# Optimization experiments

Measured on AMD Instinct MI355X. Metric: run time of the kernel, lower is better.

## Reference

```python
import jax, jax.numpy as jnp
import numpy as np

EPS_LN = 1e-5

def _layernorm(x, g, b):
    mu = x.mean(-1, keepdims=True)
    var = ((x - mu) ** 2).mean(-1, keepdims=True)
    return (x - mu) / jnp.sqrt(var + EPS_LN) * g + b


def setup_inputs() -> dict:
    key = jax.random.key(0)
    B, N, D, H = 4, 2048, 256, 4
    hid = int(D * 2.0)
    ks = jax.random.split(key, 12)
    x = jax.random.normal(ks[0], (B, N, D), jnp.float32)
    Au = jax.random.uniform(ks[1], (N, N)) < 0.004
    A = jnp.logical_or(Au, Au.T)
    A = A.at[jnp.arange(N), jnp.arange(N)].set(False)
    Af = A.astype(jnp.float32)
    deg = Af.sum(axis=1)
    L = jnp.diag(deg) - Af                      # graph Laplacian (N,N), PSD
    adjacency = Af + jnp.eye(N, dtype=jnp.float32)  # self loops so no empty softmax rows
    s = lambda k, sh, f: jax.random.normal(k, sh, jnp.float32) * f
    sc = 1.0 / np.sqrt(D)
    Wc = s(ks[2], (D, D), sc); bc = jnp.zeros((D,), jnp.float32)
    Wq = s(ks[3], (D, D), sc); Wk = s(ks[4], (D, D), sc); Wv = s(ks[5], (D, D), sc)
    Wo = s(ks[6], (D, D), sc); bo = jnp.zeros((D,), jnp.float32)
    W1 = s(ks[7], (D, hid), sc); b1 = jnp.zeros((hid,), jnp.float32)
    W2 = s(ks[8], (hid, D), 1.0 / np.sqrt(hid)); b2 = jnp.zeros((D,), jnp.float32)
    g1 = jnp.ones((D,), jnp.float32); be1 = jnp.zeros((D,), jnp.float32)
    g2 = jnp.ones((D,), jnp.float32); be2 = jnp.zeros((D,), jnp.float32)
    g3 = jnp.ones((D,), jnp.float32); be3 = jnp.zeros((D,), jnp.float32)
    return dict(x=x, L=L, adjacency=adjacency, Wc=Wc, bc=bc, g1=g1, be1=be1,
                Wq=Wq, Wk=Wk, Wv=Wv, Wo=Wo, bo=bo, g2=g2, be2=be2,
                W1=W1, b1=b1, W2=W2, b2=b2, g3=g3, be3=be3)


def reference(x, L, adjacency, Wc, bc, g1, be1, Wq, Wk, Wv, Wo, bo,
              g2, be2, W1, b1, W2, b2, g3, be3):
    B, N, D = x.shape
    H = 4
    hd = D // H
    # --- LaplacianConv: normalize L to eigenvalues in [-1, 1] ---
    eig = jnp.linalg.eigvalsh(L)               # ascending
    lam_max = eig[-1] + 1e-8
    L_norm = 2.0 * L / lam_max - jnp.eye(N, dtype=L.dtype)
    # per-channel matmul in torch == single propagation L_norm @ x
    xp = jnp.einsum('mn,bnf->bmf', L_norm, x)
    h = xp @ Wc + bc
    h = _layernorm(h, g1, be1)
    h = jax.nn.relu(h)
    x1 = h + x                                  # residual (in_dim == out_dim)
    # --- adjacency-masked multi-head attention ---
    q = (x1 @ Wq).reshape(B, N, H, hd).transpose(0, 2, 1, 3)  # (B,H,N,hd)
    k = (x1 @ Wk).reshape(B, N, H, hd).transpose(0, 2, 1, 3)
    v = (x1 @ Wv).reshape(B, N, H, hd).transpose(0, 2, 1, 3)
    scores = jnp.einsum('bhnd,bhmd->bhnm', q, k) / np.sqrt(hd).astype(np.float32)
    scores = jnp.where(adjacency[None, None] > 0, scores, jnp.float32(-1e9))
    attn = jax.nn.softmax(scores, axis=-1)
    o = jnp.einsum('bhnm,bhmd->bhnd', attn, v)
    o = o.transpose(0, 2, 1, 3).reshape(B, N, D)
    o = o @ Wo + bo
    x2 = _layernorm(x1 + o, g2, be2)
    # --- MLP ---
    m = jax.nn.gelu(x2 @ W1 + b1, approximate=False) @ W2 + b2
    return _layernorm(x2 + m, g3, be3)
```

## Files before the change

### kernel.cpp

```cpp
#include <hip/hip_runtime.h>
#include <math.h>

typedef __bf16 bf16;
typedef bf16 bf16x8 __attribute__((ext_vector_type(8)));
typedef float f32x4 __attribute__((ext_vector_type(4)));

#define LDS_PAD 40
#define SENT 2048
#define LANCZOS_M 12

__global__ __launch_bounds__(256) void k_pre(
    const float* __restrict__ Wc, const float* __restrict__ Wq, const float* __restrict__ Wk,
    const float* __restrict__ Wv, const float* __restrict__ Wo, const float* __restrict__ W1,
    const float* __restrict__ W2, const float* __restrict__ x, const float* __restrict__ adj,
    bf16* __restrict__ WcT, bf16* __restrict__ WqT, bf16* __restrict__ WkT,
    bf16* __restrict__ WvT, bf16* __restrict__ WoT, bf16* __restrict__ W1T,
    bf16* __restrict__ W2T, bf16* __restrict__ xT,
    int* __restrict__ cnt, unsigned short* __restrict__ cols)
{
    __shared__ float tile[32][33];
    int z = blockIdx.z;
    if (z == 11) {
        int flat = blockIdx.y * 16 + blockIdx.x;
        if (flat >= 512) return;
        int row = flat * 4 + (threadIdx.x >> 6);
        int lane = threadIdx.x & 63;
        int base = 0;
        for (int c0 = 0; c0 < 2048; c0 += 64) {
            float a = adj[(long)row * 2048 + c0 + lane];
            unsigned long long m = __ballot(a != 0.0f);
            if (a != 0.0f) {
                int pos = base + __popcll(m & ((1ull << lane) - 1ull));
                if (pos < 64) cols[(long)row * 64 + pos] = (unsigned short)(c0 + lane);
            }
            base += __popcll(m);
        }
        int c = base < 64 ? base : 64;
        if (lane >= c) cols[(long)row * 64 + lane] = (unsigned short)SENT;
        if (lane == 0) cnt[row] = c;
        return;
    }
    const float* src; bf16* dst; int R, C;
    switch (z) {
        case 0: src = Wc; dst = WcT; R = 256; C = 256; break;
        case 1: src = Wq; dst = WqT; R = 256; C = 256; break;
        case 2: src = Wk; dst = WkT; R = 256; C = 256; break;
        case 3: src = Wv; dst = WvT; R = 256; C = 256; break;
        case 4: src = Wo; dst = WoT; R = 256; C = 256; break;
        case 5: src = W1; dst = W1T; R = 256; C = 512; break;
        case 6: src = W2; dst = W2T; R = 512; C = 256; break;
        default: {
            int b = z - 7;
            src = x + (long)b * 2048 * 256; dst = xT + (long)b * 256 * 2048;
            R = 2048; C = 256;
        }
    }
    int c0 = blockIdx.x * 32, r0 = blockIdx.y * 32;
    if (c0 >= C || r0 >= R) return;
    int tx = threadIdx.x & 31, ty = threadIdx.x >> 5;
#pragma unroll
    for (int j = 0; j < 4; ++j)
        tile[ty + 8 * j][tx] = src[(long)(r0 + ty + 8 * j) * C + c0 + tx];
    __syncthreads();
#pragma unroll
    for (int j = 0; j < 4; ++j)
        dst[(long)(c0 + ty + 8 * j) * R + r0 + tx] = (bf16)tile[tx][ty + 8 * j];
}

__global__ __launch_bounds__(1024) void k_main(
    const int* __restrict__ cnt, const unsigned short* __restrict__ cols, float* __restrict__ lamOut,
    const float* __restrict__ L, const bf16* __restrict__ xT, float* __restrict__ xp0f)
{
    __shared__ float va[2064], vb[2064];
    __shared__ float redf[16], redf2[16];
    __shared__ int   redi[16];
    __shared__ float bcast, bcast2;
    __shared__ float alphaA[LANCZOS_M], betaA[LANCZOS_M];
    __shared__ bf16 As[64 * LDS_PAD];
    __shared__ bf16 Bs[256 * LDS_PAD];

    int t = threadIdx.x;
    if (blockIdx.x != 0) {
        int bx = blockIdx.x - 1;
        int rowBlk = (bx & 31) * 64;
        int z  = (bx >> 5) & 3;
        int ks = bx >> 7;
        long kbase = (long)ks * 1024;
        const bf16* BT = xT + (long)z * 256 * 2048;
        int w = t >> 6, lane = t & 63;
        int q = lane >> 4, l15 = lane & 15;
        int wm = w & 3, wn = w >> 2;

        f32x4 acc[4];
#pragma unroll
        for (int i = 0; i < 4; ++i) acc[i] = (f32x4){0.0f, 0.0f, 0.0f, 0.0f};

        int ar = t >> 4, ac = (t & 15) * 2;
        int br = t >> 2, bc = (t & 3) * 8;
        const float* Ap = L + (long)(rowBlk + ar) * 2048 + kbase + ac;
        const bf16* Bp = BT + (long)br * 2048 + kbase + bc;
        float2 fA = *(const float2*)Ap;
        uint4  rB = *(const uint4*)Bp;
        for (int kt = 0; kt < 1024; kt += 32) {
            __syncthreads();
            {
                union { bf16 h[2]; unsigned u; } pk;
                pk.h[0] = (bf16)fA.x; pk.h[1] = (bf16)fA.y;
                *(unsigned*)&As[ar * LDS_PAD + ac] = pk.u;
            }
            *(uint4*)&Bs[br * LDS_PAD + bc] = rB;
            __syncthreads();
            if (kt + 32 < 1024) {
                fA = *(const float2*)(Ap + kt + 32);
                rB = *(const uint4*)(Bp + kt + 32);
            }
            bf16x8 a = *(const bf16x8*)&As[(wm * 16 + l15) * LDS_PAD + q * 8];
#pragma unroll
            for (int nt = 0; nt < 4; ++nt) {
                bf16x8 b = *(const bf16x8*)&Bs[((wn * 4 + nt) * 16 + l15) * LDS_PAD + q * 8];
                acc[nt] = __builtin_amdgcn_mfma_f32_16x16x32_bf16(a, b, acc[nt], 0, 0, 0);
            }
        }
        long zRow = (long)ks * 8192 + (long)z * 2048 + rowBlk + wm * 16 + q * 4;
#pragma unroll
        for (int nt = 0; nt < 4; ++nt) {
            int col = (wn * 4 + nt) * 16 + l15;
#pragma unroll
            for (int r = 0; r < 4; ++r)
                xp0f[(zRow + r) * 256 + col] = acc[nt][r];
        }
        return;
    }
    int wid = t >> 6, lane = t & 63;
    int r0 = t, r1 = t + 1024;
    int c0 = cnt[r0], c1 = cnt[r1];
    int p0 = (c0 + 7) & ~7, p1 = (c1 + 7) & ~7;

    uint4 cr0[8], cr1[8];
#pragma unroll
    for (int j = 0; j < 8; ++j) {
        cr0[j] = ((const uint4*)(cols + (long)r0 * 64))[j];
        cr1[j] = ((const uint4*)(cols + (long)r1 * 64))[j];
    }

    int md = max(c0, c1);
#pragma unroll
    for (int off = 32; off >= 1; off >>= 1) md = max(md, __shfl_xor(md, off));
    if (lane == 0) redi[wid] = md;
    __syncthreads();
    if (t == 0) {
        int m = 0;
        for (int i = 0; i < 16; ++i) m = max(m, redi[i]);
        bcast = (float)(2 * (m - 1)) + 1.0f;
    }
    for (int i = t; i < 2048; i += 1024) {
        unsigned u = (unsigned)i * 2654435761u;
        u ^= u >> 16; u *= 2246822519u; u ^= u >> 13;
        float mag = 0.5f + (float)((u >> 9) & 1023) * (1.0f / 1024.0f);
        va[i] = (u & 1) ? mag : -mag;
    }
    if (t == 0) { va[SENT] = 0.0f; vb[SENT] = 0.0f; }
    __syncthreads();
    float hiBound = bcast;

    float d0 = va[r0], d1 = va[r1];
    float pz = d0 * d0 + d1 * d1;
#pragma unroll
    for (int off = 32; off >= 1; off >>= 1) pz += __shfl_xor(pz, off);
    if (lane == 0) redf[wid] = pz;
    __syncthreads();
    if (t == 0) { float s = 0; for (int i = 0; i < 16; ++i) s += redf[i]; bcast = s; }
    __syncthreads();
    float sc = rsqrtf(fmaxf(bcast, 1e-30f));
    d0 *= sc; d1 *= sc;
    va[r0] = d0; va[r1] = d1;
    __syncthreads();

    float* cur = va; float* nxt = vb;
    float bp = 0.0f;
    float p0r = 0.0f, p1r = 0.0f;
    for (int it = 0; it < LANCZOS_M; ++it) {
        float sum0 = 0.0f, sum1 = 0.0f;
#pragma unroll
        for (int j = 0; j < 8; ++j)
            if (j * 8 < p0) {
                uint4 q = cr0[j];
                sum0 += cur[q.x & 0xffff] + cur[q.x >> 16] + cur[q.y & 0xffff] + cur[q.y >> 16]
                      + cur[q.z & 0xffff] + cur[q.z >> 16] + cur[q.w & 0xffff] + cur[q.w >> 16];
            }
#pragma unroll
        for (int j = 0; j < 8; ++j)
            if (j * 8 < p1) {
                uint4 q = cr1[j];
                sum1 += cur[q.x & 0xffff] + cur[q.x >> 16] + cur[q.y & 0xffff] + cur[q.y >> 16]
                      + cur[q.z & 0xffff] + cur[q.z >> 16] + cur[q.w & 0xffff] + cur[q.w >> 16];
            }
        float u0 = (float)c0 * d0 - sum0 - bp * p0r;
        float u1 = (float)c1 * d1 - sum1 - bp * p1r;
        float puv = u0 * d0 + u1 * d1;
        float puu = u0 * u0 + u1 * u1;
#pragma unroll
        for (int off = 32; off >= 1; off >>= 1) {
            puv += __shfl_xor(puv, off);
            puu += __shfl_xor(puu, off);
        }
        if (lane == 0) { redf[wid] = puv; redf2[wid] = puu; }
        __syncthreads();
        if (t == 0) {
            float sv = 0, su = 0;
            for (int i = 0; i < 16; ++i) { sv += redf[i]; su += redf2[i]; }
            float b = sqrtf(fmaxf(su - sv * sv, 1e-24f));
            alphaA[it] = sv; betaA[it] = b;
            bcast = sv; bcast2 = b;
        }
        __syncthreads();
        float alpha = bcast, beta = bcast2;
        float invb = 1.0f / beta;
        float w0 = u0 - alpha * d0, w1 = u1 - alpha * d1;
        p0r = d0; p1r = d1;
        d0 = w0 * invb; d1 = w1 * invb;
        nxt[r0] = d0; nxt[r1] = d1;
        __syncthreads();
        bp = beta;
        float* tmp = cur; cur = nxt; nxt = tmp;
    }

    if (t < 64) {
        float aa[LANCZOS_M], b2[LANCZOS_M];
#pragma unroll
        for (int i = 0; i < LANCZOS_M; ++i) { aa[i] = alphaA[i]; b2[i] = betaA[i] * betaA[i]; }
        float lo = 0.0f, hi = hiBound;
        for (int round = 0; round < 4; ++round) {
            float step = (hi - lo) * (1.0f / 65.0f);
            float xm = lo + step * (float)(lane + 1);
            float dd = aa[0] - xm;
            int neg = dd < 0.0f ? 1 : 0;
#pragma unroll
            for (int i = 1; i < LANCZOS_M; ++i) {
                float ad = fmaxf(fabsf(dd), 1e-12f);
                dd = (dd < 0.0f) ? -ad : ad;
                dd = aa[i] - xm - b2[i - 1] / dd;
                neg += dd < 0.0f ? 1 : 0;
            }
            unsigned long long mb = __ballot(neg >= LANCZOS_M);
            if (mb == 0ull) {
                lo = lo + step * 64.0f;
            } else {
                int fl = (int)(__ffsll((long long)mb) - 1);
                hi = lo + step * (float)(fl + 1);
                lo = lo + step * (float)fl;
            }
        }
        if (lane == 0) lamOut[0] = 0.5f * (lo + hi) + 1e-8f;
    }
}

template <int TA, int EPI>
__global__ __launch_bounds__(256) void k_gemm(
    const bf16* __restrict__ A0, const float* __restrict__ Apa, const float* __restrict__ Apb,
    const float* __restrict__ Aaux, const bf16* __restrict__ BTg,
    float* __restrict__ outF, bf16* __restrict__ outB,
    const float* __restrict__ bias, const float* __restrict__ resid,
    const float* __restrict__ gam, const float* __restrict__ bet,
    const float* __restrict__ lamPtr,
    int K, long aZ, long btZ, long outZrows, int ldOut)
{
    __shared__ bf16 As[64 * LDS_PAD];
    __shared__ bf16 Bs[256 * LDS_PAD];

    int tid = threadIdx.x;
    int w = tid >> 6, lane = tid & 63;
    int q = lane >> 4, l15 = lane & 15;
    int rowBlk = blockIdx.x * 64;
    int colB = blockIdx.y * 256;
    const bf16* BT = BTg + (long)blockIdx.z * btZ + (long)blockIdx.y * 256 * (long)K;

    float s2 = 0.0f;
    if (TA == 2) s2 = 2.0f / lamPtr[0];

    f32x4 acc[16];
#pragma unroll
    for (int i = 0; i < 16; ++i) acc[i] = (f32x4){0.0f, 0.0f, 0.0f, 0.0f};

    int ar = tid >> 2, ac = (tid & 3) * 8;
    long abase = (long)(rowBlk + ar) * K + ac;
    const bf16* A = A0 + (long)blockIdx.z * aZ;
    const bf16* Bp = BT + (long)tid * K;

    uint4 aR;
    float4 pa0, pa1, pb0, pb1, xa0, xa1;
    uint4 bR0, bR1, bR2, bR3;
    if (TA == 1) {
        aR = *(const uint4*)(A + abase);
    } else {
        pa0 = *(const float4*)(Apa + abase);  pa1 = *(const float4*)(Apa + abase + 4);
        pb0 = *(const float4*)(Apb + abase);  pb1 = *(const float4*)(Apb + abase + 4);
        xa0 = *(const float4*)(Aaux + abase); xa1 = *(const float4*)(Aaux + abase + 4);
    }
    bR0 = ((const uint4*)Bp)[0]; bR1 = ((const uint4*)Bp)[1];
    bR2 = ((const uint4*)Bp)[2]; bR3 = ((const uint4*)Bp)[3];

    for (int kt = 0; kt < K; kt += 32) {
        __syncthreads();
        if (TA == 1) {
            *(uint4*)&As[ar * LDS_PAD + ac] = aR;
        } else {
            float pa[8] = {pa0.x, pa0.y, pa0.z, pa0.w, pa1.x, pa1.y, pa1.z, pa1.w};
            float pb[8] = {pb0.x, pb0.y, pb0.z, pb0.w, pb1.x, pb1.y, pb1.z, pb1.w};
            float xa[8] = {xa0.x, xa0.y, xa0.z, xa0.w, xa1.x, xa1.y, xa1.z, xa1.w};
            union { bf16 h[8]; uint4 u; } pk;
#pragma unroll
            for (int j = 0; j < 8; ++j) pk.h[j] = (bf16)(s2 * (pa[j] + pb[j]) - xa[j]);
            *(uint4*)&As[ar * LDS_PAD + ac] = pk.u;
        }
        {
            bf16* d = &Bs[tid * LDS_PAD];
            *(uint4*)(d + 0)  = bR0;
            *(uint4*)(d + 8)  = bR1;
            *(uint4*)(d + 16) = bR2;
            *(uint4*)(d + 24) = bR3;
        }
        __syncthreads();
        if (kt + 32 < K) {
            long nb = abase + kt + 32;
            if (TA == 1) {
                aR = *(const uint4*)(A + nb);
            } else {
                pa0 = *(const float4*)(Apa + nb);  pa1 = *(const float4*)(Apa + nb + 4);
                pb0 = *(const float4*)(Apb + nb);  pb1 = *(const float4*)(Apb + nb + 4);
                xa0 = *(const float4*)(Aaux + nb); xa1 = *(const float4*)(Aaux + nb + 4);
            }
            const bf16* p = Bp + kt + 32;
            bR0 = ((const uint4*)p)[0]; bR1 = ((const uint4*)p)[1];
            bR2 = ((const uint4*)p)[2]; bR3 = ((const uint4*)p)[3];
        }
        bf16x8 a = *(const bf16x8*)&As[(w * 16 + l15) * LDS_PAD + q * 8];
#pragma unroll
        for (int nt = 0; nt < 16; ++nt) {
            bf16x8 b = *(const bf16x8*)&Bs[(nt * 16 + l15) * LDS_PAD + q * 8];
            acc[nt] = __builtin_amdgcn_mfma_f32_16x16x32_bf16(a, b, acc[nt], 0, 0, 0);
        }
    }

    long zRow = (long)blockIdx.z * outZrows + rowBlk + w * 16 + q * 4;

    if (EPI == 0) {
#pragma unroll
        for (int nt = 0; nt < 16; ++nt) {
            int col = colB + nt * 16 + l15;
#pragma unroll
            for (int r = 0; r < 4; ++r)
                outB[(zRow + r) * (long)ldOut + col] = (bf16)acc[nt][r];
        }
        return;
    }
    if (EPI == 3) {
#pragma unroll
        for (int nt = 0; nt < 16; ++nt) {
            int col = colB + nt * 16 + l15;
            float bi = bias[col];
#pragma unroll
            for (int r = 0; r < 4; ++r) {
                float v = acc[nt][r] + bi;
                float g = 0.5f * v * (1.0f + erff(v * 0.70710678118654752440f));
                outB[(zRow + r) * (long)ldOut + col] = (bf16)g;
            }
        }
        return;
    }
    float s[4] = {0, 0, 0, 0}, sq[4] = {0, 0, 0, 0};
#pragma unroll
    for (int nt = 0; nt < 16; ++nt) {
        int col = colB + nt * 16 + l15;
        float bi = bias[col];
#pragma unroll
        for (int r = 0; r < 4; ++r) {
            float v = acc[nt][r] + bi;
            if (EPI == 2) v += resid[(zRow + r) * 256 + col];
            acc[nt][r] = v;
            s[r] += v; sq[r] += v * v;
        }
    }
#pragma unroll
    for (int off = 1; off <= 8; off <<= 1) {
#pragma unroll
        for (int r = 0; r < 4; ++r) { s[r] += __shfl_xor(s[r], off); sq[r] += __shfl_xor(sq[r], off); }
    }
    float mean[4], rstd[4];
#pragma unroll
    for (int r = 0; r < 4; ++r) {
        mean[r] = s[r] * (1.0f / 256.0f);
        float var = sq[r] * (1.0f / 256.0f) - mean[r] * mean[r];
        rstd[r] = rsqrtf(var + 1e-5f);
    }
#pragma unroll
    for (int nt = 0; nt < 16; ++nt) {
        int col = colB + nt * 16 + l15;
        float gc = gam[col], bc2 = bet[col];
#pragma unroll
        for (int r = 0; r < 4; ++r) {
            float v = (acc[nt][r] - mean[r]) * rstd[r] * gc + bc2;
            if (EPI == 1) v = fmaxf(v, 0.0f) + resid[(zRow + r) * 256 + col];
            long oi = (zRow + r) * (long)ldOut + col;
            outF[oi] = v;
            if (outB) outB[oi] = (bf16)v;
        }
    }
}

__global__ __launch_bounds__(256) void k_attn(const bf16* __restrict__ qg, const bf16* __restrict__ kg,
                                              const bf16* __restrict__ vg, bf16* __restrict__ og,
                                              const int* __restrict__ cnt, const unsigned short* __restrict__ cols)
{
    __shared__ unsigned short sc[64];
    __shared__ float sp[4][64];
    int row = blockIdx.x;
    int b = row >> 11, i = row & 2047;
    int tid = threadIdx.x, h = tid >> 6, lane = tid & 63;
    int c = cnt[i];
    if (tid < 64) sc[tid] = cols[(long)i * 64 + tid];
    __syncthreads();
    long qoff = (long)row * 256 + h * 64 + lane;
    float qd = (float)qg[qoff];
    long kvBase = (long)b * 2048;
    for (int j = 0; j < c; ++j) {
        int col = sc[j];
        float kd = (float)kg[(kvBase + col) * 256 + h * 64 + lane];
        float p = qd * kd;
#pragma unroll
        for (int off = 32; off >= 1; off >>= 1) p += __shfl_xor(p, off);
        if (lane == 0) sp[h][j] = p * 0.125f;
    }
    __syncthreads();
    float sj = (lane < c) ? sp[h][lane] : -3.0e38f;
    float mx = sj;
#pragma unroll
    for (int off = 32; off >= 1; off >>= 1) mx = fmaxf(mx, __shfl_xor(mx, off));
    float e = (lane < c) ? __expf(sj - mx) : 0.0f;
    float ssum = e;
#pragma unroll
    for (int off = 32; off >= 1; off >>= 1) ssum += __shfl_xor(ssum, off);
    if (lane < c) sp[h][lane] = e / ssum;
    __syncthreads();
    float acc = 0.0f;
    for (int j = 0; j < c; ++j) {
        int col = sc[j];
        acc += sp[h][j] * (float)vg[(kvBase + col) * 256 + h * 64 + lane];
    }
    og[qoff] = (bf16)acc;
}

extern "C" void kernel_launch(void* const* d_in, const int* in_sizes, int n_in,
                              void* d_out, int out_size, void* d_ws, size_t ws_size,
                              hipStream_t stream)
{
    const float* x   = (const float*)d_in[0];
    const float* L   = (const float*)d_in[1];
    const float* adj = (const float*)d_in[2];
    const float* Wc  = (const float*)d_in[3];
    const float* bc  = (const float*)d_in[4];
    const float* g1  = (const float*)d_in[5];
    const float* be1 = (const float*)d_in[6];
    const float* Wq  = (const float*)d_in[7];
    const float* Wk  = (const float*)d_in[8];
    const float* Wv  = (const float*)d_in[9];
    const float* Wo  = (const float*)d_in[10];
    const float* bo  = (const float*)d_in[11];
    const float* g2  = (const float*)d_in[12];
    const float* be2 = (const float*)d_in[13];
    const float* W1  = (const float*)d_in[14];
    const float* b1  = (const float*)d_in[15];
    const float* W2  = (const float*)d_in[16];
    const float* b2  = (const float*)d_in[17];
    const float* g3  = (const float*)d_in[18];
    const float* be3 = (const float*)d_in[19];
    float* out = (float*)d_out;

    char* ws = (char*)d_ws;
    size_t off = 0;
    auto alloc = [&](size_t bytes) -> void* {
        void* p = ws + off;
        off = (off + bytes + 255) & ~(size_t)255;
        return p;
    };
    float* lam           = (float*)alloc(256);
    int* cnt             = (int*)alloc(2048 * 4);
    unsigned short* cols = (unsigned short*)alloc(2048 * 64 * 2);
    bf16* WcT = (bf16*)alloc(65536 * 2);
    bf16* WqT = (bf16*)alloc(65536 * 2);
    bf16* WkT = (bf16*)alloc(65536 * 2);
    bf16* WvT = (bf16*)alloc(65536 * 2);
    bf16* WoT = (bf16*)alloc(65536 * 2);
    bf16* W1T = (bf16*)alloc(131072 * 2);
    bf16* W2T = (bf16*)alloc(131072 * 2);
    bf16* xT  = (bf16*)alloc((size_t)4 * 256 * 2048 * 2);
    float* xp0f = (float*)alloc((size_t)2 * 8192 * 256 * 4);
    float* x1f = (float*)alloc((size_t)8192 * 256 * 4);
    bf16* x1b  = (bf16*)alloc((size_t)8192 * 256 * 2);
    bf16* qb   = (bf16*)alloc((size_t)3 * 8192 * 256 * 2);
    bf16* ob   = (bf16*)alloc((size_t)8192 * 256 * 2);
    float* x2f = (float*)alloc((size_t)8192 * 256 * 4);
    bf16* x2b  = (bf16*)alloc((size_t)8192 * 256 * 2);
    bf16* m1   = (bf16*)alloc((size_t)8192 * 512 * 2);
    (void)in_sizes; (void)n_in; (void)out_size; (void)ws_size;

    dim3 blk(256);
    k_pre<<<dim3(16, 64, 12), blk, 0, stream>>>(Wc, Wq, Wk, Wv, Wo, W1, W2, x, adj,
                                                WcT, WqT, WkT, WvT, WoT, W1T, W2T, xT, cnt, cols);
    k_main<<<dim3(257), dim3(1024), 0, stream>>>(cnt, cols, lam, L, xT, xp0f);
    k_gemm<2, 1><<<dim3(128, 1, 1), blk, 0, stream>>>(
        nullptr, xp0f, xp0f + (size_t)8192 * 256, x, WcT, x1f, x1b, bc, x, g1, be1, lam,
        256, 0L, 0L, 0L, 256);
    k_gemm<1, 0><<<dim3(128, 1, 3), blk, 0, stream>>>(
        x1b, nullptr, nullptr, nullptr, WqT, nullptr, qb, nullptr, nullptr, nullptr, nullptr, nullptr,
        256, 0L, 65536L, 8192L, 256);
    bf16* kb  = qb + (size_t)8192 * 256;
    bf16* vb2 = qb + (size_t)2 * 8192 * 256;
    k_attn<<<dim3(8192), blk, 0, stream>>>(qb, kb, vb2, ob, cnt, cols);
    k_gemm<1, 2><<<dim3(128, 1, 1), blk, 0, stream>>>(
        ob, nullptr, nullptr, nullptr, WoT, x2f, x2b, bo, x1f, g2, be2, nullptr,
        256, 0L, 0L, 0L, 256);
    k_gemm<1, 3><<<dim3(128, 2, 1), blk, 0, stream>>>(
        x2b, nullptr, nullptr, nullptr, W1T, nullptr, m1, b1, nullptr, nullptr, nullptr, nullptr,
        256, 0L, 0L, 0L, 512);
    k_gemm<1, 2><<<dim3(128, 1, 1), blk, 0, stream>>>(
        m1, nullptr, nullptr, nullptr, W2T, out, nullptr, b2, x2f, g3, be3, nullptr,
        512, 0L, 0L, 0L, 256);
}
```

Measured before the change: 384.7 us.

## Halve GEMM row tile to 32 and split columns across warps

The GEMM tile shrinks from 64 to 32 rows per block, and the four warps are arranged 2x2 (row half by column half) instead of each owning 16 rows across all 256 columns. The grid doubles to 256 blocks so more of the GPU's compute units get work on these small GEMMs. Row statistics for the fused layernorm are now combined across the two column-half warps through shared memory plus an extra barrier. The cost is that each block reloads the full 256-column B tile for only 32 rows, doubling B traffic, with smaller A loads.

Result: faster. 368.5 us (-4.2%).

```diff
diff --git a/kernel.cpp b/kernel.cpp
--- a/kernel.cpp
+++ b/kernel.cpp
@@ -265,37 +265,39 @@
     const float* __restrict__ lamPtr,
     int K, long aZ, long btZ, long outZrows, int ldOut)
 {
-    __shared__ bf16 As[64 * LDS_PAD];
+    __shared__ bf16 As[32 * LDS_PAD];
     __shared__ bf16 Bs[256 * LDS_PAD];
+    __shared__ float sL[2][32], sqL[2][32];
 
     int tid = threadIdx.x;
     int w = tid >> 6, lane = tid & 63;
     int q = lane >> 4, l15 = lane & 15;
-    int rowBlk = blockIdx.x * 64;
+    int wm = w & 1, wn = w >> 1;
+    int rowBlk = blockIdx.x * 32;
     int colB = blockIdx.y * 256;
     const bf16* BT = BTg + (long)blockIdx.z * btZ + (long)blockIdx.y * 256 * (long)K;
 
     float s2 = 0.0f;
     if (TA == 2) s2 = 2.0f / lamPtr[0];
 
-    f32x4 acc[16];
-#pragma unroll
-    for (int i = 0; i < 16; ++i) acc[i] = (f32x4){0.0f, 0.0f, 0.0f, 0.0f};
-
-    int ar = tid >> 2, ac = (tid & 3) * 8;
+    f32x4 acc[8];
+#pragma unroll
+    for (int i = 0; i < 8; ++i) acc[i] = (f32x4){0.0f, 0.0f, 0.0f, 0.0f};
+
+    int ar = tid >> 3, ac = (tid & 7) * 4;
     long abase = (long)(rowBlk + ar) * K + ac;
     const bf16* A = A0 + (long)blockIdx.z * aZ;
     const bf16* Bp = BT + (long)tid * K;
 
-    uint4 aR;
-    float4 pa0, pa1, pb0, pb1, xa0, xa1;
+    uint2 aR;
+    float4 pa0, pb0, xa0;
     uint4 bR0, bR1, bR2, bR3;
     if (TA == 1) {
-        aR = *(const uint4*)(A + abase);
+        aR = *(const uint2*)(A + abase);
     } else {
-        pa0 = *(const float4*)(Apa + abase);  pa1 = *(const float4*)(Apa + abase + 4);
-        pb0 = *(const float4*)(Apb + abase);  pb1 = *(const float4*)(Apb + abase + 4);
-        xa0 = *(const float4*)(Aaux + abase); xa1 = *(const float4*)(Aaux + abase + 4);
+        pa0 = *(const float4*)(Apa + abase);
+        pb0 = *(const float4*)(Apb + abase);
+        xa0 = *(const float4*)(Aaux + abase);
     }
     bR0 = ((const uint4*)Bp)[0]; bR1 = ((const uint4*)Bp)[1];
     bR2 = ((const uint4*)Bp)[2]; bR3 = ((const uint4*)Bp)[3];
@@ -303,15 +305,15 @@
     for (int kt = 0; kt < K; kt += 32) {
         __syncthreads();
         if (TA == 1) {
-            *(uint4*)&As[ar * LDS_PAD + ac] = aR;
+            *(uint2*)&As[ar * LDS_PAD + ac] = aR;
         } else {
-            float pa[8] = {pa0.x, pa0.y, pa0.z, pa0.w, pa1.x, pa1.y, pa1.z, pa1.w};
-            float pb[8] = {pb0.x, pb0.y, pb0.z, pb0.w, pb1.x, pb1.y, pb1.z, pb1.w};
-            float xa[8] = {xa0.x, xa0.y, xa0.z, xa0.w, xa1.x, xa1.y, xa1.z, xa1.w};
-            union { bf16 h[8]; uint4 u; } pk;
-#pragma unroll
-            for (int j = 0; j < 8; ++j) pk.h[j] = (bf16)(s2 * (pa[j] + pb[j]) - xa[j]);
-            *(uint4*)&As[ar * LDS_PAD + ac] = pk.u;
+            float pa[4] = {pa0.x, pa0.y, pa0.z, pa0.w};
+            float pb[4] = {pb0.x, pb0.y, pb0.z, pb0.w};
+            float xa[4] = {xa0.x, xa0.y, xa0.z, xa0.w};
+            union { bf16 h[4]; uint2 u; } pk;
+#pragma unroll
+            for (int j = 0; j < 4; ++j) pk.h[j] = (bf16)(s2 * (pa[j] + pb[j]) - xa[j]);
+            *(uint2*)&As[ar * LDS_PAD + ac] = pk.u;
         }
         {
             bf16* d = &Bs[tid * LDS_PAD];
@@ -324,30 +326,30 @@
         if (kt + 32 < K) {
             long nb = abase + kt + 32;
             if (TA == 1) {
-                aR = *(const uint4*)(A + nb);
+                aR = *(const uint2*)(A + nb);
             } else {
-                pa0 = *(const float4*)(Apa + nb);  pa1 = *(const float4*)(Apa + nb + 4);
-                pb0 = *(const float4*)(Apb + nb);  pb1 = *(const float4*)(Apb + nb + 4);
-                xa0 = *(const float4*)(Aaux + nb); xa1 = *(const float4*)(Aaux + nb + 4);
+                pa0 = *(const float4*)(Apa + nb);
+                pb0 = *(const float4*)(Apb + nb);
+                xa0 = *(const float4*)(Aaux + nb);
             }
             const bf16* p = Bp + kt + 32;
             bR0 = ((const uint4*)p)[0]; bR1 = ((const uint4*)p)[1];
             bR2 = ((const uint4*)p)[2]; bR3 = ((const uint4*)p)[3];
         }
-        bf16x8 a = *(const bf16x8*)&As[(w * 16 + l15) * LDS_PAD + q * 8];
-#pragma unroll
-        for (int nt = 0; nt < 16; ++nt) {
-            bf16x8 b = *(const bf16x8*)&Bs[(nt * 16 + l15) * LDS_PAD + q * 8];
+        bf16x8 a = *(const bf16x8*)&As[(wm * 16 + l15) * LDS_PAD + q * 8];
+#pragma unroll
+        for (int nt = 0; nt < 8; ++nt) {
+            bf16x8 b = *(const bf16x8*)&Bs[((wn * 8 + nt) * 16 + l15) * LDS_PAD + q * 8];
             acc[nt] = __builtin_amdgcn_mfma_f32_16x16x32_bf16(a, b, acc[nt], 0, 0, 0);
         }
     }
 
-    long zRow = (long)blockIdx.z * outZrows + rowBlk + w * 16 + q * 4;
+    long zRow = (long)blockIdx.z * outZrows + rowBlk + wm * 16 + q * 4;
 
     if (EPI == 0) {
 #pragma unroll
-        for (int nt = 0; nt < 16; ++nt) {
-            int col = colB + nt * 16 + l15;
+        for (int nt = 0; nt < 8; ++nt) {
+            int col = colB + (wn * 8 + nt) * 16 + l15;
 #pragma unroll
             for (int r = 0; r < 4; ++r)
                 outB[(zRow + r) * (long)ldOut + col] = (bf16)acc[nt][r];
@@ -356,8 +358,8 @@
     }
     if (EPI == 3) {
 #pragma unroll
-        for (int nt = 0; nt < 16; ++nt) {
-            int col = colB + nt * 16 + l15;
+        for (int nt = 0; nt < 8; ++nt) {
+            int col = colB + (wn * 8 + nt) * 16 + l15;
             float bi = bias[col];
 #pragma unroll
             for (int r = 0; r < 4; ++r) {
@@ -370,8 +372,8 @@
     }
     float s[4] = {0, 0, 0, 0}, sq[4] = {0, 0, 0, 0};
 #pragma unroll
-    for (int nt = 0; nt < 16; ++nt) {
-        int col = colB + nt * 16 + l15;
+    for (int nt = 0; nt < 8; ++nt) {
+        int col = colB + (wn * 8 + nt) * 16 + l15;
         float bi = bias[col];
 #pragma unroll
         for (int r = 0; r < 4; ++r) {
@@ -386,16 +388,27 @@
 #pragma unroll
         for (int r = 0; r < 4; ++r) { s[r] += __shfl_xor(s[r], off); sq[r] += __shfl_xor(sq[r], off); }
     }
+    if (l15 == 0) {
+#pragma unroll
+        for (int r = 0; r < 4; ++r) {
+            sL[wn][wm * 16 + q * 4 + r] = s[r];
+            sqL[wn][wm * 16 + q * 4 + r] = sq[r];
+        }
+    }
+    __syncthreads();
     float mean[4], rstd[4];
 #pragma unroll
     for (int r = 0; r < 4; ++r) {
-        mean[r] = s[r] * (1.0f / 256.0f);
-        float var = sq[r] * (1.0f / 256.0f) - mean[r] * mean[r];
+        int row = wm * 16 + q * 4 + r;
+        float st = sL[0][row] + sL[1][row];
+        float sqt = sqL[0][row] + sqL[1][row];
+        mean[r] = st * (1.0f / 256.0f);
+        float var = sqt * (1.0f / 256.0f) - mean[r] * mean[r];
         rstd[r] = rsqrtf(var + 1e-5f);
     }
 #pragma unroll
-    for (int nt = 0; nt < 16; ++nt) {
-        int col = colB + nt * 16 + l15;
+    for (int nt = 0; nt < 8; ++nt) {
+        int col = colB + (wn * 8 + nt) * 16 + l15;
         float gc = gam[col], bc2 = bet[col];
 #pragma unroll
         for (int r = 0; r < 4; ++r) {
@@ -508,22 +521,22 @@
     k_pre<<<dim3(16, 64, 12), blk, 0, stream>>>(Wc, Wq, Wk, Wv, Wo, W1, W2, x, adj,
                                                 WcT, WqT, WkT, WvT, WoT, W1T, W2T, xT, cnt, cols);
     k_main<<<dim3(257), dim3(1024), 0, stream>>>(cnt, cols, lam, L, xT, xp0f);
-    k_gemm<2, 1><<<dim3(128, 1, 1), blk, 0, stream>>>(
+    k_gemm<2, 1><<<dim3(256, 1, 1), blk, 0, stream>>>(
         nullptr, xp0f, xp0f + (size_t)8192 * 256, x, WcT, x1f, x1b, bc, x, g1, be1, lam,
         256, 0L, 0L, 0L, 256);
-    k_gemm<1, 0><<<dim3(128, 1, 3), blk, 0, stream>>>(
+    k_gemm<1, 0><<<dim3(256, 1, 3), blk, 0, stream>>>(
         x1b, nullptr, nullptr, nullptr, WqT, nullptr, qb, nullptr, nullptr, nullptr, nullptr, nullptr,
         256, 0L, 65536L, 8192L, 256);
     bf16* kb  = qb + (size_t)8192 * 256;
     bf16* vb2 = qb + (size_t)2 * 8192 * 256;
     k_attn<<<dim3(8192), blk, 0, stream>>>(qb, kb, vb2, ob, cnt, cols);
-    k_gemm<1, 2><<<dim3(128, 1, 1), blk, 0, stream>>>(
+    k_gemm<1, 2><<<dim3(256, 1, 1), blk, 0, stream>>>(
         ob, nullptr, nullptr, nullptr, WoT, x2f, x2b, bo, x1f, g2, be2, nullptr,
         256, 0L, 0L, 0L, 256);
-    k_gemm<1, 3><<<dim3(128, 2, 1), blk, 0, stream>>>(
+    k_gemm<1, 3><<<dim3(256, 2, 1), blk, 0, stream>>>(
         x2b, nullptr, nullptr, nullptr, W1T, nullptr, m1, b1, nullptr, nullptr, nullptr, nullptr,
         256, 0L, 0L, 0L, 512);
-    k_gemm<1, 2><<<dim3(128, 1, 1), blk, 0, stream>>>(
+    k_gemm<1, 2><<<dim3(256, 1, 1), blk, 0, stream>>>(
         m1, nullptr, nullptr, nullptr, W2T, out, nullptr, b2, x2f, g3, be3, nullptr,
         512, 0L, 0L, 0L, 256);
 }
```
